# Kernel optimization log

Measured on AMD Instinct MI355X. Metric: run time of the kernel, lower is better.

The kernel has to match this reference:

```python
import jax, jax.numpy as jnp
import numpy as np

C = 256
CQK = C // 8  # 32

def setup_inputs() -> dict:
    key = jax.random.key(0)
    ks = jax.random.split(key, 8)
    B, H, W = 8, 64, 64
    x = jax.random.normal(ks[0], (B, C, H, W), dtype=jnp.float32)
    y = jax.random.normal(ks[1], (B, C, H, W), dtype=jnp.float32)
    s = 1.0 / np.sqrt(C)
    Wq = jax.random.normal(ks[2], (CQK, C), dtype=jnp.float32) * s
    bq = jnp.zeros((CQK,), dtype=jnp.float32)
    Wk = jax.random.normal(ks[3], (CQK, C), dtype=jnp.float32) * s
    bk = jnp.zeros((CQK,), dtype=jnp.float32)
    Wv = jax.random.normal(ks[4], (C, C), dtype=jnp.float32) * s
    bv = jnp.zeros((C,), dtype=jnp.float32)
    return {"x": x, "y": y, "Wq": Wq, "bq": bq, "Wk": Wk, "bk": bk, "Wv": Wv, "bv": bv}

def reference(x, y, Wq, bq, Wk, bk, Wv, bv):
    B, Cc, H, W = x.shape
    HW = H * W
    xf = x.reshape(B, Cc, HW)  # [B,C,HW]
    yf = y.reshape(B, Cc, HW)
    # 1x1 convs == per-pixel linear projections
    Q = jnp.einsum('oc,bcn->bno', Wq, xf) + bq          # [B,HW,CQK]
    K = jnp.einsum('oc,bcn->bon', Wk, yf) + bk[:, None]  # [B,CQK,HW]
    V = jnp.einsum('oc,bcn->bon', Wv, yf) + bv[:, None]  # [B,C,HW]
    attn = jax.nn.softmax(jnp.einsum('bnd,bdm->bnm', Q, K), axis=-1)  # [B,HW,HW]
    out = jnp.einsum('bcm,bnm->bcn', V, attn)  # V @ attn^T -> [B,C,HW]
    return out.reshape(B, Cc, H, W)
```

## Files before the change

### kernel.cpp

```cpp
#include <hip/hip_runtime.h>

typedef unsigned short u16;
typedef _Float16 f16;
typedef __attribute__((ext_vector_type(8))) short v8s;
typedef __attribute__((ext_vector_type(4))) short v4s;
typedef __attribute__((ext_vector_type(8))) f16   v8h;
typedef __attribute__((ext_vector_type(4))) float v4f;
typedef __attribute__((ext_vector_type(16))) float v16f;
typedef __attribute__((ext_vector_type(4))) unsigned v4u;

#define NB   8
#define NC   256
#define DQK  32
#define NPIX 4096

__device__ __forceinline__ u16 f2bf(float f) {
  unsigned u = __builtin_bit_cast(unsigned, f);
  u += 0x7FFFu + ((u >> 16) & 1u);
  return (u16)(u >> 16);
}
__device__ __forceinline__ u16 f2h(float f) {
  return __builtin_bit_cast(u16, (f16)f);
}
__device__ __forceinline__ unsigned cvt_pk_bf16(float lo, float hi) {
  unsigned r;
  asm("v_cvt_pk_bf16_f32 %0, %1, %2" : "=v"(r) : "v"(lo), "v"(hi));
  return r;
}
__device__ __forceinline__ float fast_exp2(float x) {
  float r;
  asm("v_exp_f32 %0, %1" : "=v"(r) : "v"(x));
  return r;
}

__global__ __launch_bounds__(256)
void convert_w(const float* __restrict__ Wq, const float* __restrict__ Wk,
               const float* __restrict__ Wv,
               u16* __restrict__ Whq, u16* __restrict__ Whk, u16* __restrict__ Whv) {
  int i = blockIdx.x * 256 + threadIdx.x;
  if (i < 8192)       Whq[i]         = f2h(Wq[i]);
  else if (i < 16384) Whk[i - 8192]  = f2h(Wk[i - 8192]);
  else                Whv[i - 16384] = f2h(Wv[i - 16384]);
}

__global__ __launch_bounds__(256)
void xpose(const float* __restrict__ x, const float* __restrict__ y,
           u16* __restrict__ xt, u16* __restrict__ yt) {
  const float* __restrict__ src = blockIdx.y ? y : x;
  u16* __restrict__ dst         = blockIdx.y ? yt : xt;
  const int bid = blockIdx.x;
  const int b  = bid >> 8;
  const int c0 = ((bid >> 6) & 3) * 64;
  const int n0 = (bid & 63) * 64;
  __shared__ u16 T[64][66];
  const int t = threadIdx.x, nl = t & 63, cq = t >> 6;
  const float* __restrict__ s = src + ((size_t)b << 20) + (size_t)c0 * NPIX + n0;
#pragma unroll
  for (int i = 0; i < 16; ++i) {
    int c = cq * 16 + i;
    T[c][nl] = f2h(s[(size_t)c * NPIX + nl]);
  }
  __syncthreads();
  u16* __restrict__ d = dst + ((size_t)b << 20) + (size_t)n0 * NC + c0;
#pragma unroll
  for (int i = 0; i < 2; ++i) {
    int nr = (t >> 3) + 32 * i, c8 = (t & 7) * 8;
    v8s v;
#pragma unroll
    for (int j = 0; j < 8; ++j) v[j] = (short)T[c8 + j][nr];
    *(v8s*)(d + (size_t)nr * NC + c8) = v;
  }
}

__global__ __launch_bounds__(256)
void proj_mfma(const u16* __restrict__ xt, const u16* __restrict__ yt,
               const u16* __restrict__ Whq, const float* __restrict__ bq,
               const u16* __restrict__ Whk, const float* __restrict__ bk,
               const u16* __restrict__ Whv, const float* __restrict__ bv,
               u16* __restrict__ Qb, u16* __restrict__ Kb, u16* __restrict__ Vt) {
  const int tid = threadIdx.x, w = tid >> 6, lane = tid & 63;
  const int lr = lane & 15, quad = lane >> 4;
  const int b = blockIdx.x & 7;
  const int n0 = (blockIdx.x >> 3) * 64;
  const int n = n0 + w * 16 + lr;
  const size_t bn = ((size_t)b << 12) + n;

  v8h xb[8], yb[8];
  const u16* xp = xt + bn * NC + quad * 8;
  const u16* yp = yt + bn * NC + quad * 8;
#pragma unroll
  for (int t = 0; t < 8; ++t) {
    xb[t] = *(const v8h*)(xp + 32 * t);
    yb[t] = *(const v8h*)(yp + 32 * t);
  }

#pragma unroll
  for (int ot = 0; ot < 2; ++ot) {
    v4f aq = {0.f, 0.f, 0.f, 0.f}, ak = {0.f, 0.f, 0.f, 0.f};
#pragma unroll
    for (int t = 0; t < 8; ++t) {
      v8h wq = *(const v8h*)(Whq + (ot * 16 + lr) * 256 + quad * 8 + 32 * t);
      v8h wk = *(const v8h*)(Whk + (ot * 16 + lr) * 256 + quad * 8 + 32 * t);
      aq = __builtin_amdgcn_mfma_f32_16x16x32_f16(wq, xb[t], aq, 0, 0, 0);
      ak = __builtin_amdgcn_mfma_f32_16x16x32_f16(wk, yb[t], ak, 0, 0, 0);
    }
    v4f bqv = *(const v4f*)(bq + ot * 16 + quad * 4);
    v4f bkv = *(const v4f*)(bk + ot * 16 + quad * 4);
    v4s q4, k4;
#pragma unroll
    for (int r = 0; r < 4; ++r) {
      q4[r] = (short)f2h(aq[r] + bqv[r]);
      k4[r] = (short)f2h(ak[r] + bkv[r]);
    }
    *(v4s*)(Qb + bn * DQK + ot * 16 + quad * 4) = q4;
    *(v4s*)(Kb + bn * DQK + ot * 16 + quad * 4) = k4;
  }

  for (int vt = 0; vt < 16; ++vt) {
    v4f av = {0.f, 0.f, 0.f, 0.f};
#pragma unroll
    for (int t = 0; t < 8; ++t) {
      v8h wv = *(const v8h*)(Whv + (vt * 16 + lr) * 256 + quad * 8 + 32 * t);
      av = __builtin_amdgcn_mfma_f32_16x16x32_f16(wv, yb[t], av, 0, 0, 0);
    }
#pragma unroll
    for (int r = 0; r < 4; ++r) {
      int o = vt * 16 + quad * 4 + r;
      size_t off = ((((size_t)b * 64 + (n >> 6)) * 32 + (o >> 5) * 4 + ((n >> 4) & 3)) * 64
                    + ((n >> 3) & 1) * 32 + (o & 31)) * 8 + (n & 7);
      Vt[off] = f2bf(av[r] + bv[o]);
    }
  }
}

#define L2E  1.44269504f
#define SHFT -48.0f

#define PACK_TILE(S, PBLO, PBHI)                                              \
  {                                                                           \
    float e0  = fast_exp2(fmaf(S[0],  L2E, SHFT));                            \
    float e1  = fast_exp2(fmaf(S[1],  L2E, SHFT));                            \
    float e2  = fast_exp2(fmaf(S[2],  L2E, SHFT));                            \
    float e3  = fast_exp2(fmaf(S[3],  L2E, SHFT));                            \
    float e4  = fast_exp2(fmaf(S[4],  L2E, SHFT));                            \
    float e5  = fast_exp2(fmaf(S[5],  L2E, SHFT));                            \
    float e6  = fast_exp2(fmaf(S[6],  L2E, SHFT));                            \
    float e7  = fast_exp2(fmaf(S[7],  L2E, SHFT));                            \
    float e8  = fast_exp2(fmaf(S[8],  L2E, SHFT));                            \
    float e9  = fast_exp2(fmaf(S[9],  L2E, SHFT));                            \
    float e10 = fast_exp2(fmaf(S[10], L2E, SHFT));                            \
    float e11 = fast_exp2(fmaf(S[11], L2E, SHFT));                            \
    float e12 = fast_exp2(fmaf(S[12], L2E, SHFT));                            \
    float e13 = fast_exp2(fmaf(S[13], L2E, SHFT));                            \
    float e14 = fast_exp2(fmaf(S[14], L2E, SHFT));                            \
    float e15 = fast_exp2(fmaf(S[15], L2E, SHFT));                            \
    lsum += (((e0 + e1) + (e2 + e3)) + ((e4 + e5) + (e6 + e7)))               \
          + (((e8 + e9) + (e10 + e11)) + ((e12 + e13) + (e14 + e15)));        \
    unsigned u00 = cvt_pk_bf16(e0,  e1),  u01 = cvt_pk_bf16(e2,  e3);         \
    unsigned u10 = cvt_pk_bf16(e4,  e5),  u11 = cvt_pk_bf16(e6,  e7);         \
    unsigned u20 = cvt_pk_bf16(e8,  e9),  u21 = cvt_pk_bf16(e10, e11);        \
    unsigned u30 = cvt_pk_bf16(e12, e13), u31 = cvt_pk_bf16(e14, e15);        \
    asm("v_permlane32_swap_b32 %0, %1" : "+v"(u00), "+v"(u10));               \
    asm("v_permlane32_swap_b32 %0, %1" : "+v"(u01), "+v"(u11));               \
    asm("v_permlane32_swap_b32 %0, %1" : "+v"(u20), "+v"(u30));               \
    asm("v_permlane32_swap_b32 %0, %1" : "+v"(u21), "+v"(u31));               \
    PBLO = __builtin_bit_cast(v8s, (v4u){u00, u01, u10, u11});                \
    PBHI = __builtin_bit_cast(v8s, (v4u){u20, u21, u30, u31});                \
  }

__global__ __launch_bounds__(512, 2)
void attn_kernel(const u16* __restrict__ Qb, const u16* __restrict__ Kb,
                 const u16* __restrict__ Vt, float* __restrict__ out) {
  __shared__ __attribute__((aligned(16))) u16 Vb[4][32][64][8];
  __shared__ float Ls2[4][32];

  const int tid  = threadIdx.x;
  const int w    = tid >> 6;
  const int lane = tid & 63;
  const int l31  = lane & 31;
  const int wq   = w & 3;
  const int g    = w >> 2;
  const int bufbase = g * 2;

  const int b  = blockIdx.x & 7;
  const int q0 = (blockIdx.x >> 3) << 7;
  const int qw = q0 + wq * 32;

  const int h = lane >> 5;
  const u16* Qp = Qb + ((size_t)b * NPIX + qw + l31) * DQK + h * 8;
  const v8h qf0 = *(const v8h*)(Qp);
  const v8h qf1 = *(const v8h*)(Qp + 16);

  const u16* Kp = Kb + ((size_t)b * NPIX + l31) * DQK + h * 8 + (size_t)g * 32 * 2048;

  const u16* Vg = Vt + ((size_t)b << 20) + (size_t)lane * 8 + (size_t)g * 32 * 16384;

  v16f acc[8];
#pragma unroll
  for (int i = 0; i < 8; ++i) acc[i] = (v16f){};
  float lsum = 0.f;
  const v16f vz = (v16f){};

#pragma unroll
  for (int j = 0; j < 8; ++j) {
    const int f = wq * 8 + j;
    __builtin_amdgcn_global_load_lds(
        (const __attribute__((address_space(1))) unsigned*)(Vg + (size_t)f * 512),
        (__attribute__((address_space(3))) unsigned*)(&Vb[bufbase][f][0][0]), 16, 0, 0);
  }
  v8h kc0 = *(const v8h*)(Kp);
  v8h kc1 = *(const v8h*)(Kp + 16);
  v8h kc2 = *(const v8h*)(Kp + 1024);
  v8h kc3 = *(const v8h*)(Kp + 1040);
  v8h kn0 = kc0, kn1 = kc1, kn2 = kc2, kn3 = kc3;

  v8s pB0, pB1, pB2, pB3;
  {
    v16f sA = __builtin_amdgcn_mfma_f32_32x32x16_f16(kc0, qf0, vz, 0, 0, 0);
    sA = __builtin_amdgcn_mfma_f32_32x32x16_f16(kc1, qf1, sA, 0, 0, 0);
    v16f sB = __builtin_amdgcn_mfma_f32_32x32x16_f16(kc2, qf0, vz, 0, 0, 0);
    sB = __builtin_amdgcn_mfma_f32_32x32x16_f16(kc3, qf1, sB, 0, 0, 0);
    PACK_TILE(sA, pB0, pB1);
    PACK_TILE(sB, pB2, pB3);
  }
  {
    const u16* kp1 = Kp + 2048;
    kc0 = *(const v8h*)(kp1);
    kc1 = *(const v8h*)(kp1 + 16);
    kc2 = *(const v8h*)(kp1 + 1024);
    kc3 = *(const v8h*)(kp1 + 1040);
  }

#pragma unroll 1
  for (int it = 0; it < 32; ++it) {
    const int pp = it & 1;
    __builtin_amdgcn_sched_barrier(0);
    if (it < 31) {
      asm volatile("s_waitcnt vmcnt(4)" ::: "memory");
    } else {
      asm volatile("s_waitcnt vmcnt(0)" ::: "memory");
    }
    __builtin_amdgcn_s_barrier();
    __builtin_amdgcn_sched_barrier(0);

    if (it < 31) {
#pragma unroll
      for (int j = 0; j < 8; ++j) {
        const int f = wq * 8 + j;
        __builtin_amdgcn_global_load_lds(
            (const __attribute__((address_space(1))) unsigned*)(Vg + ((size_t)(it + 1) * 32 + f) * 512),
            (__attribute__((address_space(3))) unsigned*)(&Vb[bufbase + (pp ^ 1)][f][0][0]), 16, 0, 0);
      }
    }

    __builtin_amdgcn_s_setprio(1);
#pragma unroll
    for (int ct = 0; ct < 8; ++ct) {
      v8s vf0 = *(const v8s*)(&Vb[bufbase + pp][ct * 4 + 0][lane][0]);
      v8s vf1 = *(const v8s*)(&Vb[bufbase + pp][ct * 4 + 1][lane][0]);
      v8s vf2 = *(const v8s*)(&Vb[bufbase + pp][ct * 4 + 2][lane][0]);
      v8s vf3 = *(const v8s*)(&Vb[bufbase + pp][ct * 4 + 3][lane][0]);
      acc[ct] = __builtin_amdgcn_mfma_f32_32x32x16_bf16(vf0, pB0, acc[ct], 0, 0, 0);
      acc[ct] = __builtin_amdgcn_mfma_f32_32x32x16_bf16(vf1, pB1, acc[ct], 0, 0, 0);
      acc[ct] = __builtin_amdgcn_mfma_f32_32x32x16_bf16(vf2, pB2, acc[ct], 0, 0, 0);
      acc[ct] = __builtin_amdgcn_mfma_f32_32x32x16_bf16(vf3, pB3, acc[ct], 0, 0, 0);
    }
    __builtin_amdgcn_s_setprio(0);

    if (it < 31) {
      v16f sA = __builtin_amdgcn_mfma_f32_32x32x16_f16(kc0, qf0, vz, 0, 0, 0);
      sA = __builtin_amdgcn_mfma_f32_32x32x16_f16(kc1, qf1, sA, 0, 0, 0);
      v16f sB = __builtin_amdgcn_mfma_f32_32x32x16_f16(kc2, qf0, vz, 0, 0, 0);
      sB = __builtin_amdgcn_mfma_f32_32x32x16_f16(kc3, qf1, sB, 0, 0, 0);
      if (it < 30) {
        const u16* kp2 = Kp + (size_t)(it + 2) * 2048;
        kn0 = *(const v8h*)(kp2);
        kn1 = *(const v8h*)(kp2 + 16);
        kn2 = *(const v8h*)(kp2 + 1024);
        kn3 = *(const v8h*)(kp2 + 1040);
      }
      PACK_TILE(sA, pB0, pB1);
      PACK_TILE(sB, pB2, pB3);
      kc0 = kn0; kc1 = kn1; kc2 = kn2; kc3 = kn3;
    }
  }

  lsum += __shfl_xor(lsum, 32);

  __syncthreads();
  float* Cb = (float*)&Vb[0][0][0][0];
  if (w >= 4) {
    const int w4 = w - 4;
#pragma unroll
    for (int ct = 0; ct < 8; ++ct)
#pragma unroll
      for (int k = 0; k < 4; ++k) {
        v4f c = {acc[ct][k * 4 + 0], acc[ct][k * 4 + 1],
                 acc[ct][k * 4 + 2], acc[ct][k * 4 + 3]};
        *(v4f*)(Cb + (((w4 * 32 + ct * 4 + k) * 64 + lane) << 2)) = c;
      }
    if (lane < 32) Ls2[w4][l31] = lsum;
  }
  __syncthreads();
  if (w < 4) {
    const float linv = 1.0f / (lsum + Ls2[w][l31]);
#pragma unroll
    for (int ct = 0; ct < 8; ++ct)
#pragma unroll
      for (int k = 0; k < 4; ++k) {
        v4f c = *(const v4f*)(Cb + (((w * 32 + ct * 4 + k) * 64 + lane) << 2));
        acc[ct][k * 4 + 0] += c[0]; acc[ct][k * 4 + 1] += c[1];
        acc[ct][k * 4 + 2] += c[2]; acc[ct][k * 4 + 3] += c[3];
      }

    float* op = out + (size_t)b * NC * NPIX + q0 + wq * 32 + l31;
#pragma unroll
    for (int ct = 0; ct < 8; ++ct)
#pragma unroll
      for (int r = 0; r < 16; ++r) {
        const int ch = ct * 32 + (r & 3) + ((r >> 2) << 3) + (h << 2);
        op[(size_t)ch * NPIX] = acc[ct][r] * linv;
      }
  }
}

extern "C" void kernel_launch(void* const* d_in, const int* in_sizes, int n_in,
                              void* d_out, int out_size, void* d_ws, size_t ws_size,
                              hipStream_t stream) {
  const float* x  = (const float*)d_in[0];
  const float* y  = (const float*)d_in[1];
  const float* Wq = (const float*)d_in[2];
  const float* bq = (const float*)d_in[3];
  const float* Wk = (const float*)d_in[4];
  const float* bk = (const float*)d_in[5];
  const float* Wv = (const float*)d_in[6];
  const float* bv = (const float*)d_in[7];
  float* out = (float*)d_out;

  u16* Qb  = (u16*)d_ws;
  u16* Kb  = Qb + (size_t)NB * NPIX * DQK;
  u16* Vt  = Kb + (size_t)NB * NPIX * DQK;
  u16* xt  = Vt + (size_t)NB * NC * NPIX;
  u16* yt  = xt + (size_t)NB * NPIX * NC;
  u16* Whq = yt + (size_t)NB * NPIX * NC;
  u16* Whk = Whq + 32 * 256;
  u16* Whv = Whk + 32 * 256;

  hipLaunchKernelGGL(convert_w, dim3(320), dim3(256), 0, stream, Wq, Wk, Wv, Whq, Whk, Whv);
  hipLaunchKernelGGL(xpose, dim3(2048, 2), dim3(256), 0, stream, x, y, xt, yt);
  hipLaunchKernelGGL(proj_mfma, dim3(512), dim3(256), 0, stream,
                     xt, yt, Whq, bq, Whk, bk, Whv, bv, Qb, Kb, Vt);
  hipLaunchKernelGGL(attn_kernel, dim3(256), dim3(512), 0, stream, Qb, Kb, Vt, out);
}
```

Baseline: 250.6 us.

## Fuse transpose/fp16 conversion into projection kernel via LDS staging

Removes the separate xpose kernel and its fp16 transposed xt/yt intermediates. The projection kernel now reads fp32 x/y directly in 64-channel slices, converts and transposes them through shared memory, and accumulates Q/K/V projections across four channel chunks. This saves a kernel launch and a round trip of the transposed activations through global memory. In exchange it holds 20 accumulator vectors in registers and adds per-chunk block barriers.

```diff
diff --git a/kernel.cpp b/kernel.cpp
--- a/kernel.cpp
+++ b/kernel.cpp
@@ -44,91 +44,93 @@
 }
 
 __global__ __launch_bounds__(256)
-void xpose(const float* __restrict__ x, const float* __restrict__ y,
-           u16* __restrict__ xt, u16* __restrict__ yt) {
-  const float* __restrict__ src = blockIdx.y ? y : x;
-  u16* __restrict__ dst         = blockIdx.y ? yt : xt;
-  const int bid = blockIdx.x;
-  const int b  = bid >> 8;
-  const int c0 = ((bid >> 6) & 3) * 64;
-  const int n0 = (bid & 63) * 64;
-  __shared__ u16 T[64][66];
-  const int t = threadIdx.x, nl = t & 63, cq = t >> 6;
-  const float* __restrict__ s = src + ((size_t)b << 20) + (size_t)c0 * NPIX + n0;
-#pragma unroll
-  for (int i = 0; i < 16; ++i) {
-    int c = cq * 16 + i;
-    T[c][nl] = f2h(s[(size_t)c * NPIX + nl]);
-  }
-  __syncthreads();
-  u16* __restrict__ d = dst + ((size_t)b << 20) + (size_t)n0 * NC + c0;
-#pragma unroll
-  for (int i = 0; i < 2; ++i) {
-    int nr = (t >> 3) + 32 * i, c8 = (t & 7) * 8;
-    v8s v;
-#pragma unroll
-    for (int j = 0; j < 8; ++j) v[j] = (short)T[c8 + j][nr];
-    *(v8s*)(d + (size_t)nr * NC + c8) = v;
-  }
-}
-
-__global__ __launch_bounds__(256)
-void proj_mfma(const u16* __restrict__ xt, const u16* __restrict__ yt,
-               const u16* __restrict__ Whq, const float* __restrict__ bq,
-               const u16* __restrict__ Whk, const float* __restrict__ bk,
-               const u16* __restrict__ Whv, const float* __restrict__ bv,
-               u16* __restrict__ Qb, u16* __restrict__ Kb, u16* __restrict__ Vt) {
+void proj_fused(const float* __restrict__ x, const float* __restrict__ y,
+                const u16* __restrict__ Whq, const float* __restrict__ bq,
+                const u16* __restrict__ Whk, const float* __restrict__ bk,
+                const u16* __restrict__ Whv, const float* __restrict__ bv,
+                u16* __restrict__ Qb, u16* __restrict__ Kb, u16* __restrict__ Vt) {
+  __shared__ u16 Tx[64][66], Ty[64][66];
+
   const int tid = threadIdx.x, w = tid >> 6, lane = tid & 63;
   const int lr = lane & 15, quad = lane >> 4;
+  const int nl = lane;
   const int b = blockIdx.x & 7;
   const int n0 = (blockIdx.x >> 3) * 64;
   const int n = n0 + w * 16 + lr;
   const size_t bn = ((size_t)b << 12) + n;
-
-  v8h xb[8], yb[8];
-  const u16* xp = xt + bn * NC + quad * 8;
-  const u16* yp = yt + bn * NC + quad * 8;
-#pragma unroll
-  for (int t = 0; t < 8; ++t) {
-    xb[t] = *(const v8h*)(xp + 32 * t);
-    yb[t] = *(const v8h*)(yp + 32 * t);
+  const int col = w * 16 + lr;
+
+  v4f aq[2], ak[2], av[16];
+#pragma unroll
+  for (int ot = 0; ot < 2; ++ot) { aq[ot] = (v4f){0.f,0.f,0.f,0.f}; ak[ot] = (v4f){0.f,0.f,0.f,0.f}; }
+#pragma unroll
+  for (int vt = 0; vt < 16; ++vt) av[vt] = (v4f){0.f,0.f,0.f,0.f};
+
+#pragma unroll 1
+  for (int cs = 0; cs < 4; ++cs) {
+    if (cs) __syncthreads();
+    const float* __restrict__ xs = x + ((size_t)b << 20) + (size_t)(cs * 64) * NPIX + n0;
+    const float* __restrict__ ys = y + ((size_t)b << 20) + (size_t)(cs * 64) * NPIX + n0;
+#pragma unroll
+    for (int i = 0; i < 16; ++i) {
+      int c = w * 16 + i;
+      Tx[c][nl] = f2h(xs[(size_t)c * NPIX + nl]);
+      Ty[c][nl] = f2h(ys[(size_t)c * NPIX + nl]);
+    }
+    __syncthreads();
+
+    v8s tx0, tx1, ty0, ty1;
+#pragma unroll
+    for (int j = 0; j < 8; ++j) {
+      tx0[j] = (short)Tx[quad * 8 + j][col];
+      tx1[j] = (short)Tx[32 + quad * 8 + j][col];
+      ty0[j] = (short)Ty[quad * 8 + j][col];
+      ty1[j] = (short)Ty[32 + quad * 8 + j][col];
+    }
+    const v8h xb0 = __builtin_bit_cast(v8h, tx0);
+    const v8h xb1 = __builtin_bit_cast(v8h, tx1);
+    const v8h yb0 = __builtin_bit_cast(v8h, ty0);
+    const v8h yb1 = __builtin_bit_cast(v8h, ty1);
+
+#pragma unroll
+    for (int ot = 0; ot < 2; ++ot) {
+      const u16* wqp = Whq + (ot * 16 + lr) * 256 + cs * 64 + quad * 8;
+      const u16* wkp = Whk + (ot * 16 + lr) * 256 + cs * 64 + quad * 8;
+      aq[ot] = __builtin_amdgcn_mfma_f32_16x16x32_f16(*(const v8h*)(wqp),      xb0, aq[ot], 0, 0, 0);
+      aq[ot] = __builtin_amdgcn_mfma_f32_16x16x32_f16(*(const v8h*)(wqp + 32), xb1, aq[ot], 0, 0, 0);
+      ak[ot] = __builtin_amdgcn_mfma_f32_16x16x32_f16(*(const v8h*)(wkp),      yb0, ak[ot], 0, 0, 0);
+      ak[ot] = __builtin_amdgcn_mfma_f32_16x16x32_f16(*(const v8h*)(wkp + 32), yb1, ak[ot], 0, 0, 0);
+    }
+#pragma unroll
+    for (int vt = 0; vt < 16; ++vt) {
+      const u16* wvp = Whv + (vt * 16 + lr) * 256 + cs * 64 + quad * 8;
+      av[vt] = __builtin_amdgcn_mfma_f32_16x16x32_f16(*(const v8h*)(wvp),      yb0, av[vt], 0, 0, 0);
+      av[vt] = __builtin_amdgcn_mfma_f32_16x16x32_f16(*(const v8h*)(wvp + 32), yb1, av[vt], 0, 0, 0);
+    }
   }
 
 #pragma unroll
   for (int ot = 0; ot < 2; ++ot) {
-    v4f aq = {0.f, 0.f, 0.f, 0.f}, ak = {0.f, 0.f, 0.f, 0.f};
-#pragma unroll
-    for (int t = 0; t < 8; ++t) {
-      v8h wq = *(const v8h*)(Whq + (ot * 16 + lr) * 256 + quad * 8 + 32 * t);
-      v8h wk = *(const v8h*)(Whk + (ot * 16 + lr) * 256 + quad * 8 + 32 * t);
-      aq = __builtin_amdgcn_mfma_f32_16x16x32_f16(wq, xb[t], aq, 0, 0, 0);
-      ak = __builtin_amdgcn_mfma_f32_16x16x32_f16(wk, yb[t], ak, 0, 0, 0);
-    }
     v4f bqv = *(const v4f*)(bq + ot * 16 + quad * 4);
     v4f bkv = *(const v4f*)(bk + ot * 16 + quad * 4);
     v4s q4, k4;
 #pragma unroll
     for (int r = 0; r < 4; ++r) {
-      q4[r] = (short)f2h(aq[r] + bqv[r]);
-      k4[r] = (short)f2h(ak[r] + bkv[r]);
+      q4[r] = (short)f2h(aq[ot][r] + bqv[r]);
+      k4[r] = (short)f2h(ak[ot][r] + bkv[r]);
     }
     *(v4s*)(Qb + bn * DQK + ot * 16 + quad * 4) = q4;
     *(v4s*)(Kb + bn * DQK + ot * 16 + quad * 4) = k4;
   }
 
+#pragma unroll
   for (int vt = 0; vt < 16; ++vt) {
-    v4f av = {0.f, 0.f, 0.f, 0.f};
-#pragma unroll
-    for (int t = 0; t < 8; ++t) {
-      v8h wv = *(const v8h*)(Whv + (vt * 16 + lr) * 256 + quad * 8 + 32 * t);
-      av = __builtin_amdgcn_mfma_f32_16x16x32_f16(wv, yb[t], av, 0, 0, 0);
-    }
 #pragma unroll
     for (int r = 0; r < 4; ++r) {
       int o = vt * 16 + quad * 4 + r;
       size_t off = ((((size_t)b * 64 + (n >> 6)) * 32 + (o >> 5) * 4 + ((n >> 4) & 3)) * 64
                     + ((n >> 3) & 1) * 32 + (o & 31)) * 8 + (n & 7);
-      Vt[off] = f2bf(av[r] + bv[o]);
+      Vt[off] = f2bf(av[vt][r] + bv[o]);
     }
   }
 }
@@ -340,15 +342,12 @@
   u16* Qb  = (u16*)d_ws;
   u16* Kb  = Qb + (size_t)NB * NPIX * DQK;
   u16* Vt  = Kb + (size_t)NB * NPIX * DQK;
-  u16* xt  = Vt + (size_t)NB * NC * NPIX;
-  u16* yt  = xt + (size_t)NB * NPIX * NC;
-  u16* Whq = yt + (size_t)NB * NPIX * NC;
+  u16* Whq = Vt + (size_t)NB * NC * NPIX;
   u16* Whk = Whq + 32 * 256;
   u16* Whv = Whk + 32 * 256;
 
   hipLaunchKernelGGL(convert_w, dim3(320), dim3(256), 0, stream, Wq, Wk, Wv, Whq, Whk, Whv);
-  hipLaunchKernelGGL(xpose, dim3(2048, 2), dim3(256), 0, stream, x, y, xt, yt);
-  hipLaunchKernelGGL(proj_mfma, dim3(512), dim3(256), 0, stream,
-                     xt, yt, Whq, bq, Whk, bk, Whv, bv, Qb, Kb, Vt);
+  hipLaunchKernelGGL(proj_fused, dim3(512), dim3(256), 0, stream,
+                     x, y, Whq, bq, Whk, bk, Whv, bv, Qb, Kb, Vt);
   hipLaunchKernelGGL(attn_kernel, dim3(256), dim3(512), 0, stream, Qb, Kb, Vt, out);
 }
```

Result: faster. 237.0 us (-5.4%).
